# Kernel tuning notes

Measured on AMD Instinct MI355X. Metric: run time of the kernel, lower is better.

Reference implementation:

```python
import jax, jax.numpy as jnp
import numpy as np

N = 50000       # nodes
E = 500000      # edges
IN = 128        # in_channels
H = 128         # hidden_channels
R = 8           # num_relations


def setup_inputs() -> dict:
    key = jax.random.key(0)
    ks = jax.random.split(key, 12)
    s_in = 1.0 / np.sqrt(IN)
    s_h = 1.0 / np.sqrt(H)
    return {
        "x": jax.random.normal(ks[0], (N, IN), dtype=jnp.float32),
        "edge_index": jax.random.randint(ks[1], (2, E), 0, N),
        "edge_type": jax.random.randint(ks[2], (E,), 0, R),
        "W1": jax.random.normal(ks[3], (R, IN, H), dtype=jnp.float32) * s_in,
        "root1": jax.random.normal(ks[4], (IN, H), dtype=jnp.float32) * s_in,
        "b1": jnp.zeros((H,), dtype=jnp.float32),
        "W2": jax.random.normal(ks[5], (R, H, H), dtype=jnp.float32) * s_h,
        "root2": jax.random.normal(ks[6], (H, H), dtype=jnp.float32) * s_h,
        "b2": jnp.zeros((H,), dtype=jnp.float32),
        "Wc": jax.random.normal(ks[7], (H, 1), dtype=jnp.float32) * s_h,
        "bc": jnp.zeros((1,), dtype=jnp.float32),
    }


def rgcn_layer(x, W, root, bias, src, dst, etype, num_nodes):
    """PyG RGCNConv (no basis decomposition, aggr='mean', root weight + bias):
    out[i] = x[i] @ root + bias + sum_r mean_{(j->i) in rel r} x[j] @ W[r]
    """
    out = x @ root + bias
    for r in range(W.shape[0]):  # small fixed relation count
        mask = (etype == r).astype(x.dtype)          # [E]
        xr = x @ W[r]                                 # [N, out]
        msg = xr[src] * mask[:, None]                 # gather + mask, [E, out]
        s = jax.ops.segment_sum(msg, dst, num_segments=num_nodes)   # [N, out]
        cnt = jax.ops.segment_sum(mask, dst, num_segments=num_nodes)  # [N]
        out = out + s / jnp.maximum(cnt, 1.0)[:, None]
    return out


def reference(x, edge_index, edge_type, W1, root1, b1, W2, root2, b2, Wc, bc):
    src, dst = edge_index[0], edge_index[1]
    h = jax.nn.relu(rgcn_layer(x, W1, root1, b1, src, dst, edge_type, x.shape[0]))
    # dropout p=0.2 is identity in eval mode
    h = jax.nn.relu(rgcn_layer(h, W2, root2, b2, src, dst, edge_type, x.shape[0]))
    return (h @ Wc + bc)[:, 0]  # squeeze(-1) -> [N]
```

## Files before the change

kernel.cpp:

```cpp
#include <hip/hip_runtime.h>

#define Hd 128
#define LDA 136
#define ZW 1152
#define ZW2 576
#define MAXDEG 64

typedef __attribute__((ext_vector_type(8))) short short8;
typedef __attribute__((ext_vector_type(4))) float f32x4;
typedef __attribute__((ext_vector_type(4))) unsigned int u32x4;

__device__ __forceinline__ unsigned short f2bf(float f) {
    union { float f; unsigned u; } v; v.f = f;
    unsigned r = v.u + 0x7FFFu + ((v.u >> 16) & 1u);
    return (unsigned short)(r >> 16);
}

__global__ __launch_bounds__(256) void prep_kernel(const float* __restrict__ x,
                                                   unsigned short* __restrict__ xbf, int n4,
                                                   const float* __restrict__ root1,
                                                   const float* __restrict__ W1,
                                                   const float* __restrict__ root2,
                                                   const float* __restrict__ W2,
                                                   unsigned short* __restrict__ Bt,
                                                   const int* __restrict__ src,
                                                   const int* __restrict__ dstp,
                                                   const int* __restrict__ et, int E,
                                                   int* __restrict__ deg,
                                                   unsigned int* __restrict__ epk,
                                                   unsigned long long* __restrict__ ovf,
                                                   int* __restrict__ ovfc) {
    const int tid = threadIdx.x;
    if (blockIdx.x < 18) {
        __shared__ float S[32 * 129];
        const int b = blockIdx.x;
        const float* Ws;
        if (b == 0)       Ws = root1;
        else if (b < 9)   Ws = W1 + (size_t)(b - 1) * 16384;
        else if (b == 9)  Ws = root2;
        else              Ws = W2 + (size_t)(b - 10) * 16384;
        unsigned short* Bd = Bt + (size_t)b * 16384;
        for (int s = 0; s < 4; ++s) {
            __syncthreads();
#pragma unroll
            for (int i = 0; i < 16; ++i) {
                int idx = i * 256 + tid;
                int k = idx >> 7, n = idx & 127;
                S[k * 129 + n] = Ws[(size_t)(32 * s + k) * 128 + n];
            }
            __syncthreads();
#pragma unroll
            for (int i = 0; i < 16; ++i) {
                int idx = i * 256 + tid;
                int n = idx >> 5, kk = idx & 31;
                int k = 32 * s + kk;
                int kp = (b >= 9) ? (((k & 15) << 3) | (k >> 4)) : k;
                Bd[n * 128 + kp] = f2bf(S[kk * 129 + n]);
            }
        }
    } else if (blockIdx.x < 18 + 512) {
        const int stride = 512 * 256;
        for (int i = (blockIdx.x - 18) * 256 + tid; i < n4; i += stride) {
            float4 v = ((const float4*)x)[i];
            ushort4 o;
            o.x = f2bf(v.x); o.y = f2bf(v.y); o.z = f2bf(v.z); o.w = f2bf(v.w);
            ((ushort4*)xbf)[i] = o;
        }
    } else {
        int e = (blockIdx.x - 530) * 256 + tid;
        if (e < E) {
            int r = et[e];
            int d = dstp[e];
            int idx = atomicAdd(&deg[d], 1);
            unsigned pay = ((unsigned)src[e] << 3) | (unsigned)r;
            if (idx < MAXDEG) epk[(size_t)d * MAXDEG + idx] = pay;
            else {
                int o = atomicAdd(ovfc, 1);
                ovf[o] = ((unsigned long long)(unsigned)d << 32) | pay;
            }
        }
    }
}

__global__ __launch_bounds__(256, 2) void gemm_z(const unsigned short* __restrict__ A,
                                                 const unsigned short* __restrict__ Bt9,
                                                 unsigned short* __restrict__ z, int M) {
    __shared__ __align__(16) unsigned short As[128 * LDA];
    __shared__ __align__(16) unsigned short Bs[128 * LDA];
    const int tid = threadIdx.x;
    const int mtile = blockIdx.x / 9, ctile = blockIdx.x % 9;
    const int rowBase = mtile * 128;
    const int wave = tid >> 6, lane = tid & 63;
    const int lm = lane & 15, lk = (lane >> 4) * 8;
    const unsigned short* Btt = Bt9 + (size_t)ctile * 16384;

#pragma unroll
    for (int i = 0; i < 8; ++i) {
        int idx = i * 256 + tid;
        int r = idx >> 4, c16 = idx & 15;
        int grow = rowBase + r; if (grow >= M) grow = M - 1;
        *(float4*)&As[r * LDA + c16 * 8] = *(const float4*)&A[(size_t)grow * Hd + c16 * 8];
        *(float4*)&Bs[r * LDA + c16 * 8] = *(const float4*)&Btt[idx * 8];
    }

    f32x4 acc[2][8];
#pragma unroll
    for (int mt = 0; mt < 2; ++mt)
#pragma unroll
        for (int nt = 0; nt < 8; ++nt) acc[mt][nt] = (f32x4){0.f, 0.f, 0.f, 0.f};

    __syncthreads();
#pragma unroll
    for (int ks = 0; ks < 4; ++ks) {
        const int k0 = ks * 32 + lk;
        short8 af0 = *(const short8*)&As[(wave * 32 + lm) * LDA + k0];
        short8 af1 = *(const short8*)&As[(wave * 32 + 16 + lm) * LDA + k0];
#pragma unroll
        for (int nt = 0; nt < 8; ++nt) {
            short8 bf = *(const short8*)&Bs[(nt * 16 + lm) * LDA + k0];
            acc[0][nt] = __builtin_amdgcn_mfma_f32_16x16x32_bf16(af0, bf, acc[0][nt], 0, 0, 0);
            acc[1][nt] = __builtin_amdgcn_mfma_f32_16x16x32_bf16(af1, bf, acc[1][nt], 0, 0, 0);
        }
    }

    const int rquad = (lane >> 4) * 4;
#pragma unroll
    for (int mt = 0; mt < 2; ++mt)
#pragma unroll
        for (int reg = 0; reg < 4; ++reg) {
            int row = rowBase + wave * 32 + mt * 16 + rquad + reg;
            if (row >= M) continue;
            u32x4 q;
#pragma unroll
            for (int j = 0; j < 4; ++j) {
                unsigned lo = f2bf(acc[mt][2 * j][reg]);
                unsigned hi = f2bf(acc[mt][2 * j + 1][reg]);
                q[j] = lo | (hi << 16);
            }
            *(u32x4*)((char*)z + (size_t)row * (ZW * 2) + ctile * 256 + lm * 16) = q;
        }
}

__global__ __launch_bounds__(256) void gather_out(const unsigned short* __restrict__ z,
                                                  const int* __restrict__ deg,
                                                  const unsigned int* __restrict__ epk,
                                                  const unsigned long long* __restrict__ ovf,
                                                  const int* __restrict__ ovfc,
                                                  const float* __restrict__ bias,
                                                  const float* __restrict__ Wc,
                                                  const float* __restrict__ bc,
                                                  unsigned short* __restrict__ outb,
                                                  float* __restrict__ outf,
                                                  int N, int mode) {
    const int lane = threadIdx.x & 63;
    const int node = (int)((blockIdx.x * 256 + threadIdx.x) >> 6);
    if (node >= N) return;
    const unsigned int* z32 = (const unsigned int*)z;

    unsigned int vr = z32[(size_t)node * ZW2 + lane];
    int dt = __builtin_amdgcn_readfirstlane(deg[node]);
    unsigned int ep_v = epk[(size_t)node * MAXDEG + lane];
    const int degc = (dt < MAXDEG) ? dt : MAXDEG;
    const int rel_l = (int)(ep_v & 7u);
    const bool valid = lane < degc;

    int cnt_l = 0;
#pragma unroll
    for (int r = 0; r < 8; ++r) {
        unsigned long long m = __ballot(valid && (rel_l == r));
        int c = (int)__popcll(m);
        if (lane == r) cnt_l = c;
    }
    if (dt > MAXDEG) {
        int oc = __builtin_amdgcn_readfirstlane(ovfc[0]);
        for (int j = 0; j < oc; ++j) {
            unsigned long long v = ovf[j];
            if ((int)(v >> 32) == node && lane == (int)(v & 7u)) cnt_l++;
        }
    }
    float winv = 1.0f / (float)((cnt_l < 1) ? 1 : cnt_l);

    float t0 = 0.f, t1 = 0.f;
#pragma unroll 1
    for (int g = 0; g < degc; g += 16) {
        unsigned vb[16];
        float wb[16];
#pragma unroll
        for (int k = 0; k < 16; ++k) {
            int i = g + k;
            int ic = (i < degc) ? i : (degc - 1);
            unsigned pk = (unsigned)__builtin_amdgcn_readfirstlane(__shfl((int)ep_v, ic));
            int rel = (int)(pk & 7u);
            unsigned base = (pk >> 3) * ZW2 + (unsigned)(rel + 1) * 64;
            vb[k] = z32[(size_t)base + lane];
            wb[k] = __shfl(winv, rel);
        }
#pragma unroll
        for (int k = 0; k < 16; ++k) {
            if (g + k < degc) {
                t0 += wb[k] * __uint_as_float(vb[k] << 16);
                t1 += wb[k] * __uint_as_float(vb[k] & 0xffff0000u);
            }
        }
    }
    if (dt > MAXDEG) {
        int oc = __builtin_amdgcn_readfirstlane(ovfc[0]);
        for (int j = 0; j < oc; ++j) {
            unsigned long long v = ovf[j];
            if ((int)(v >> 32) == node) {
                unsigned pk = (unsigned)(v & 0xffffffffu);
                int rel = (int)(pk & 7u);
                unsigned base = (pk >> 3) * ZW2 + (unsigned)(rel + 1) * 64;
                unsigned u = z32[(size_t)base + lane];
                float w = __shfl(winv, rel);
                t0 += w * __uint_as_float(u << 16);
                t1 += w * __uint_as_float(u & 0xffff0000u);
            }
        }
    }

    const int c0 = (((2 * lane) & 7) << 4) + (lane >> 2);
    t0 += __uint_as_float(vr << 16) + bias[c0];
    t1 += __uint_as_float(vr & 0xffff0000u) + bias[c0 + 16];
    t0 = fmaxf(t0, 0.f);
    t1 = fmaxf(t1, 0.f);

    if (mode == 1) {
        unsigned lo = f2bf(t0), hi = f2bf(t1);
        ((unsigned int*)outb)[(size_t)node * 64 + lane] = lo | (hi << 16);
    } else {
        float s = t0 * Wc[c0] + t1 * Wc[c0 + 16];
        s += __shfl_xor(s, 1);
        s += __shfl_xor(s, 2);
        s += __shfl_xor(s, 4);
        s += __shfl_xor(s, 8);
        s += __shfl_xor(s, 16);
        s += __shfl_xor(s, 32);
        if (lane == 0) outf[node] = s + bc[0];
    }
}

extern "C" void kernel_launch(void* const* d_in, const int* in_sizes, int n_in,
                              void* d_out, int out_size, void* d_ws, size_t ws_size,
                              hipStream_t stream) {
    const float* x     = (const float*)d_in[0];
    const int*   ei    = (const int*)d_in[1];
    const int*   et    = (const int*)d_in[2];
    const float* W1    = (const float*)d_in[3];
    const float* root1 = (const float*)d_in[4];
    const float* b1    = (const float*)d_in[5];
    const float* W2    = (const float*)d_in[6];
    const float* root2 = (const float*)d_in[7];
    const float* b2    = (const float*)d_in[8];
    const float* Wc    = (const float*)d_in[9];
    const float* bc    = (const float*)d_in[10];
    float* out = (float*)d_out;

    const int N = in_sizes[0] / Hd;
    const int E = in_sizes[2];
    const int* src  = ei;
    const int* dstp = ei + E;

    const size_t NH = (size_t)N * Hd;

    size_t off = 0;
    auto carve = [&](size_t bytes) -> char* {
        char* p = (char*)d_ws + off;
        off += (bytes + 255) & ~(size_t)255;
        return p;
    };
    unsigned short* xbf  = (unsigned short*)carve(NH * 2);
    unsigned short* z    = (unsigned short*)carve((size_t)N * ZW * 2);
    unsigned short* Bt   = (unsigned short*)carve((size_t)2 * 9 * 16384 * 2);
    int*            deg  = (int*)carve((size_t)N * 4);
    int*            ovfc = (int*)carve(4);
    unsigned long long* ovf = (unsigned long long*)carve((size_t)E * 8);
    unsigned int*   epk  = (unsigned int*)carve((size_t)N * MAXDEG * 4);
    if (off > ws_size) return;

    size_t zspan = (size_t)((char*)ovfc - (char*)deg) + 256;
    hipMemsetAsync(deg, 0, zspan, stream);

    const int n4 = (int)(NH / 4);
    const int eBlocks = (E + 255) / 256;
    prep_kernel<<<530 + eBlocks, 256, 0, stream>>>(x, xbf, n4, root1, W1, root2, W2, Bt,
                                                   src, dstp, et, E, deg, epk, ovf, ovfc);

    const int Mtiles = (N + 127) / 128;
    const int nodeBlocks = (N + 3) / 4;

    gemm_z<<<Mtiles * 9, 256, 0, stream>>>(xbf, Bt, z, N);
    gather_out<<<nodeBlocks, 256, 0, stream>>>(z, deg, epk, ovf, ovfc, b1, nullptr, nullptr,
                                               xbf, nullptr, N, 1);
    gemm_z<<<Mtiles * 9, 256, 0, stream>>>(xbf, Bt + (size_t)9 * 16384, z, N);
    gather_out<<<nodeBlocks, 256, 0, stream>>>(z, deg, epk, ovf, ovfc, b2, Wc, bc,
                                               nullptr, out, N, 2);
}
```

Measured before the change: 246.1 us.

## Split gather across half-waves with 8-byte loads and swizzle GEMM blocks per XCD

```diff
diff --git a/kernel.cpp b/kernel.cpp
--- a/kernel.cpp
+++ b/kernel.cpp
@@ -88,7 +88,13 @@
     __shared__ __align__(16) unsigned short As[128 * LDA];
     __shared__ __align__(16) unsigned short Bs[128 * LDA];
     const int tid = threadIdx.x;
-    const int mtile = blockIdx.x / 9, ctile = blockIdx.x % 9;
+
+    const int nwg = gridDim.x;
+    const int nq = nwg >> 3, rr = nwg & 7;
+    const int xcd = blockIdx.x & 7, bix = blockIdx.x >> 3;
+    const int swz = (xcd < rr ? xcd * (nq + 1) : rr * (nq + 1) + (xcd - rr) * nq) + bix;
+    const int mtile = swz / 9, ctile = swz % 9;
+
     const int rowBase = mtile * 128;
     const int wave = tid >> 6, lane = tid & 63;
     const int lm = lane & 15, lk = (lane >> 4) * 8;
@@ -130,14 +136,14 @@
         for (int reg = 0; reg < 4; ++reg) {
             int row = rowBase + wave * 32 + mt * 16 + rquad + reg;
             if (row >= M) continue;
-            u32x4 q;
+            u32x4 qv;
 #pragma unroll
             for (int j = 0; j < 4; ++j) {
                 unsigned lo = f2bf(acc[mt][2 * j][reg]);
                 unsigned hi = f2bf(acc[mt][2 * j + 1][reg]);
-                q[j] = lo | (hi << 16);
-            }
-            *(u32x4*)((char*)z + (size_t)row * (ZW * 2) + ctile * 256 + lm * 16) = q;
+                qv[j] = lo | (hi << 16);
+            }
+            *(u32x4*)((char*)z + (size_t)row * (ZW * 2) + ctile * 256 + lm * 16) = qv;
         }
 }
 
@@ -156,8 +162,10 @@
     const int node = (int)((blockIdx.x * 256 + threadIdx.x) >> 6);
     if (node >= N) return;
     const unsigned int* z32 = (const unsigned int*)z;
-
-    unsigned int vr = z32[(size_t)node * ZW2 + lane];
+    const int half = lane >> 5;
+    const int q = lane & 31;
+
+    uint2 vr = *(const uint2*)(z32 + (size_t)node * ZW2 + 2 * q);
     int dt = __builtin_amdgcn_readfirstlane(deg[node]);
     unsigned int ep_v = epk[(size_t)node * MAXDEG + lane];
     const int degc = (dt < MAXDEG) ? dt : MAXDEG;
@@ -180,27 +188,27 @@
     }
     float winv = 1.0f / (float)((cnt_l < 1) ? 1 : cnt_l);
 
-    float t0 = 0.f, t1 = 0.f;
+    float t0 = 0.f, t1 = 0.f, t2 = 0.f, t3 = 0.f;
 #pragma unroll 1
     for (int g = 0; g < degc; g += 16) {
-        unsigned vb[16];
-        float wb[16];
-#pragma unroll
-        for (int k = 0; k < 16; ++k) {
-            int i = g + k;
+        uint2 vb[8];
+        float wb[8];
+#pragma unroll
+        for (int k = 0; k < 8; ++k) {
+            int i = g + 2 * k + half;
             int ic = (i < degc) ? i : (degc - 1);
-            unsigned pk = (unsigned)__builtin_amdgcn_readfirstlane(__shfl((int)ep_v, ic));
+            unsigned pk = (unsigned)__shfl((int)ep_v, ic);
             int rel = (int)(pk & 7u);
             unsigned base = (pk >> 3) * ZW2 + (unsigned)(rel + 1) * 64;
-            vb[k] = z32[(size_t)base + lane];
-            wb[k] = __shfl(winv, rel);
-        }
-#pragma unroll
-        for (int k = 0; k < 16; ++k) {
-            if (g + k < degc) {
-                t0 += wb[k] * __uint_as_float(vb[k] << 16);
-                t1 += wb[k] * __uint_as_float(vb[k] & 0xffff0000u);
-            }
+            vb[k] = *(const uint2*)(z32 + (size_t)base + 2 * q);
+            wb[k] = (i < degc) ? __shfl(winv, rel) : 0.f;
+        }
+#pragma unroll
+        for (int k = 0; k < 8; ++k) {
+            t0 += wb[k] * __uint_as_float(vb[k].x << 16);
+            t1 += wb[k] * __uint_as_float(vb[k].x & 0xffff0000u);
+            t2 += wb[k] * __uint_as_float(vb[k].y << 16);
+            t3 += wb[k] * __uint_as_float(vb[k].y & 0xffff0000u);
         }
     }
     if (dt > MAXDEG) {
@@ -211,31 +219,48 @@
                 unsigned pk = (unsigned)(v & 0xffffffffu);
                 int rel = (int)(pk & 7u);
                 unsigned base = (pk >> 3) * ZW2 + (unsigned)(rel + 1) * 64;
-                unsigned u = z32[(size_t)base + lane];
+                uint2 u = *(const uint2*)(z32 + (size_t)base + 2 * q);
                 float w = __shfl(winv, rel);
-                t0 += w * __uint_as_float(u << 16);
-                t1 += w * __uint_as_float(u & 0xffff0000u);
-            }
-        }
-    }
-
-    const int c0 = (((2 * lane) & 7) << 4) + (lane >> 2);
-    t0 += __uint_as_float(vr << 16) + bias[c0];
-    t1 += __uint_as_float(vr & 0xffff0000u) + bias[c0 + 16];
-    t0 = fmaxf(t0, 0.f);
-    t1 = fmaxf(t1, 0.f);
+                if (half == 0) {
+                    t0 += w * __uint_as_float(u.x << 16);
+                    t1 += w * __uint_as_float(u.x & 0xffff0000u);
+                    t2 += w * __uint_as_float(u.y << 16);
+                    t3 += w * __uint_as_float(u.y & 0xffff0000u);
+                }
+            }
+        }
+    }
+
+    t0 += __shfl_xor(t0, 32);
+    t1 += __shfl_xor(t1, 32);
+    t2 += __shfl_xor(t2, 32);
+    t3 += __shfl_xor(t3, 32);
+
+    const int p0 = 4 * q;
+    const int c0 = ((p0 & 7) << 4) + (p0 >> 3);
+    const int c1 = (((p0 + 1) & 7) << 4) + ((p0 + 1) >> 3);
+    const int c2 = (((p0 + 2) & 7) << 4) + ((p0 + 2) >> 3);
+    const int c3 = (((p0 + 3) & 7) << 4) + ((p0 + 3) >> 3);
+
+    t0 = fmaxf(t0 + __uint_as_float(vr.x << 16)         + bias[c0], 0.f);
+    t1 = fmaxf(t1 + __uint_as_float(vr.x & 0xffff0000u) + bias[c1], 0.f);
+    t2 = fmaxf(t2 + __uint_as_float(vr.y << 16)         + bias[c2], 0.f);
+    t3 = fmaxf(t3 + __uint_as_float(vr.y & 0xffff0000u) + bias[c3], 0.f);
 
     if (mode == 1) {
-        unsigned lo = f2bf(t0), hi = f2bf(t1);
-        ((unsigned int*)outb)[(size_t)node * 64 + lane] = lo | (hi << 16);
+        if (half == 0) {
+            uint2 o;
+            o.x = (unsigned)f2bf(t0) | ((unsigned)f2bf(t1) << 16);
+            o.y = (unsigned)f2bf(t2) | ((unsigned)f2bf(t3) << 16);
+            *(uint2*)((unsigned int*)outb + (size_t)node * 64 + 2 * q) = o;
+        }
     } else {
-        float s = t0 * Wc[c0] + t1 * Wc[c0 + 16];
+        float s = t0 * Wc[c0] + t1 * Wc[c1] + t2 * Wc[c2] + t3 * Wc[c3];
         s += __shfl_xor(s, 1);
         s += __shfl_xor(s, 2);
         s += __shfl_xor(s, 4);
         s += __shfl_xor(s, 8);
         s += __shfl_xor(s, 16);
-        s += __shfl_xor(s, 32);
         if (lane == 0) outf[node] = s + bc[0];
     }
 }
```

Result: faster. 231.9 us (-5.8%).
